# Performance work log

Measured on AMD Instinct MI355X. Metric: run time of the kernel, lower is better.

Reference implementation:

```python
import jax, jax.numpy as jnp
import numpy as np

DIM = 2048
HEADS = 16
HDIM = DIM // HEADS  # 128
B = 1
F, HG, WG = 5, 20, 32
L = F * HG * WG  # 3200
EPS = 1e-6
MAXPOS = 1024
C = HDIM // 2  # 64 rotary pairs
S0 = C - 2 * (C // 3)  # 22 (frame band)
S1 = C // 3            # 21 (height band)


def _rope_tables():
    # Matches Wan rope_params: per-band inverse-freq tables, angle = pos * inv_freq.
    pos = np.arange(MAXPOS, dtype=np.float64)
    chunks = []
    for s in (S0, S1, S1):
        d = 2 * s
        inv = 1.0 / (10000.0 ** (np.arange(0, d, 2, dtype=np.float64) / d))
        chunks.append(np.outer(pos, inv))
    ang = np.concatenate(chunks, axis=1)  # [MAXPOS, C]
    return np.cos(ang).astype(np.float32), np.sin(ang).astype(np.float32)


def setup_inputs() -> dict:
    key = jax.random.key(0)
    ks = jax.random.split(key, 6)
    sc = 1.0 / np.sqrt(DIM)
    fc, fs = _rope_tables()
    return {
        'x': jax.random.normal(ks[0], (B, L, DIM), dtype=jnp.float32),
        'wq': jax.random.normal(ks[1], (DIM, DIM), dtype=jnp.float32) * sc,
        'bq': jnp.zeros((DIM,), jnp.float32),
        'wk': jax.random.normal(ks[2], (DIM, DIM), dtype=jnp.float32) * sc,
        'bk': jnp.zeros((DIM,), jnp.float32),
        'wv': jax.random.normal(ks[3], (DIM, DIM), dtype=jnp.float32) * sc,
        'bv': jnp.zeros((DIM,), jnp.float32),
        'wo': jax.random.normal(ks[4], (DIM, DIM), dtype=jnp.float32) * sc,
        'bo': jnp.zeros((DIM,), jnp.float32),
        'norm_q_w': jnp.ones((DIM,), jnp.float32),
        'norm_k_w': jnp.ones((DIM,), jnp.float32),
        'freqs_cos': jnp.asarray(fc),
        'freqs_sin': jnp.asarray(fs),
    }


def _grid_freqs(tab):
    # Split bands and broadcast over the (F, HG, WG) grid -> [L, C]
    bf, bh, bw = tab[:, :S0], tab[:, S0:S0 + S1], tab[:, S0 + S1:]
    gf = jnp.broadcast_to(bf[:F, None, None, :], (F, HG, WG, S0))
    gh = jnp.broadcast_to(bh[None, :HG, None, :], (F, HG, WG, S1))
    gw = jnp.broadcast_to(bw[None, None, :WG, :], (F, HG, WG, S1))
    return jnp.concatenate([gf, gh, gw], axis=-1).reshape(L, C)


def reference(x, wq, bq, wk, bk, wv, bv, wo, bo, norm_q_w, norm_k_w, freqs_cos, freqs_sin):
    def rms(t, w):
        return t * jax.lax.rsqrt(jnp.mean(t * t, axis=-1, keepdims=True) + EPS) * w

    q = rms(x @ wq.T + bq, norm_q_w).reshape(B, L, HEADS, HDIM)
    k = rms(x @ wk.T + bk, norm_k_w).reshape(B, L, HEADS, HDIM)
    v = (x @ wv.T + bv).reshape(B, L, HEADS, HDIM)

    fc = _grid_freqs(freqs_cos)  # [L, C]
    fs = _grid_freqs(freqs_sin)

    def rope(t):
        tr = t.reshape(B, L, HEADS, C, 2)
        xr, xi = tr[..., 0], tr[..., 1]
        c = fc[None, :, None, :]
        s = fs[None, :, None, :]
        return jnp.stack([xr * c - xi * s, xr * s + xi * c], axis=-1).reshape(B, L, HEADS, HDIM)

    q = rope(q)
    k = rope(k)

    scores = jnp.einsum('blhd,bmhd->bhlm', q, k) / jnp.sqrt(jnp.float32(HDIM))
    attn = jax.nn.softmax(scores, axis=-1)
    out = jnp.einsum('bhlm,bmhd->blhd', attn, v).reshape(B, L, DIM)
    return out @ wo.T + bo
```

## Files before the change

kernel.cpp:

```cpp
#include <hip/hip_runtime.h>

typedef unsigned short u16;
typedef unsigned int u32;
typedef __attribute__((ext_vector_type(4))) float f32x4;
typedef __attribute__((ext_vector_type(8))) short bf16x8;
typedef __attribute__((ext_vector_type(8))) u16 u16x8;
typedef __attribute__((ext_vector_type(4))) u16 u16x4;
typedef __attribute__((ext_vector_type(4))) u32 u32x4;

#define GLOB_AS __attribute__((address_space(1)))
#define LDS_AS  __attribute__((address_space(3)))

__device__ __forceinline__ void gload_lds16(const void* g, void* l) {
  __builtin_amdgcn_global_load_lds((const GLOB_AS void*)g, (LDS_AS void*)l, 16, 0, 0);
}

__device__ __forceinline__ u16 f2bf(float f) {
  u32 u = __builtin_bit_cast(u32, f);
  u += 0x7fffu + ((u >> 16) & 1u);
  return (u16)(u >> 16);
}

__device__ __forceinline__ float bf2f(u16 b) {
  u32 u = (u32)b << 16;
  return __builtin_bit_cast(float, u);
}

#define MFMA16(a, b, c) __builtin_amdgcn_mfma_f32_16x16x32_bf16(a, b, c, 0, 0, 0)

__global__ __launch_bounds__(256) void cast_all(const float* __restrict__ x,
                                                const float* __restrict__ wq,
                                                const float* __restrict__ wk,
                                                const float* __restrict__ wv,
                                                const float* __restrict__ wo,
                                                u16* __restrict__ xb, u16* __restrict__ wqb,
                                                u16* __restrict__ wkb, u16* __restrict__ wvb,
                                                u16* __restrict__ wob) {
  int i = blockIdx.x * 256 + threadIdx.x;
  const float* s;
  u16* d;
  int off;
  if (i < 819200)       { s = x;  d = xb;  off = i; }
  else if (i < 1343488) { s = wq; d = wqb; off = i - 819200; }
  else if (i < 1867776) { s = wk; d = wkb; off = i - 1343488; }
  else if (i < 2392064) { s = wv; d = wvb; off = i - 1867776; }
  else                  { s = wo; d = wob; off = i - 2392064; }
  f32x4 a = ((const f32x4*)s)[2 * off], b = ((const f32x4*)s)[2 * off + 1];
  u16x8 o;
  o[0] = f2bf(a[0]); o[1] = f2bf(a[1]); o[2] = f2bf(a[2]); o[3] = f2bf(a[3]);
  o[4] = f2bf(b[0]); o[5] = f2bf(b[1]); o[6] = f2bf(b[2]); o[7] = f2bf(b[3]);
  ((u16x8*)d)[off] = o;
}

#define GEMM_BODY(C_WRITE)                                                        \
  f32x4 acc[4][4] = {};                                                           \
  const u32 dstoff = wave * 2048 + lane * 8;       \
  int gsb = 0;                                                                    \
  const u16* Agp = Ag;                                                            \
  const u16* Bgp = Bg;                                                            \
  _Pragma("unroll") for (int pf = 0; pf < 2; ++pf) {                              \
    u16* ad = &As[gsb][0] + dstoff;                                               \
    u16* bd = &Bs[gsb][0] + dstoff;                                               \
    gload_lds16(Agp, ad);                                                         \
    gload_lds16(Agp + (size_t)8 * K + d4, ad + 512);                              \
    gload_lds16(Agp + (size_t)16 * K, ad + 1024);                                 \
    gload_lds16(Agp + (size_t)24 * K + d4, ad + 1536);                            \
    gload_lds16(Bgp, bd);                                                         \
    gload_lds16(Bgp + (size_t)8 * K + d4, bd + 512);                              \
    gload_lds16(Bgp + (size_t)16 * K, bd + 1024);                                 \
    gload_lds16(Bgp + (size_t)24 * K + d4, bd + 1536);                            \
    Agp += 64;                                                                    \
    Bgp += 64;                                                                    \
    gsb ^= 1;                                                                     \
  }                                                                               \
  for (int it = 0; it < 32; ++it) {                                               \
    const int buf = it & 1;                                                       \
    if (it < 31)                                                                  \
      asm volatile("s_waitcnt vmcnt(8)" ::: "memory");                            \
    else                                                                          \
      asm volatile("s_waitcnt vmcnt(0)" ::: "memory");                            \
    __builtin_amdgcn_s_barrier();                                                 \
    _Pragma("unroll") for (int kk = 0; kk < 64; kk += 32) {                       \
      bf16x8 af[4], bfr[4];                                                       \
      _Pragma("unroll") for (int mi = 0; mi < 4; mi++)                            \
          af[mi] = *(const bf16x8*)&As[buf][((wr + mi * 16 + li) >> 1) * 128 +    \
              ((((kk >> 3) + lg + 8 * (li & 1)) ^ (li >> 1)) * 8)];               \
      _Pragma("unroll") for (int ni = 0; ni < 4; ni++)                            \
          bfr[ni] = *(const bf16x8*)&Bs[buf][((wc + ni * 16 + li) >> 1) * 128 +   \
              ((((kk >> 3) + lg + 8 * (li & 1)) ^ (li >> 1)) * 8)];               \
      _Pragma("unroll") for (int mi = 0; mi < 4; mi++)                            \
          _Pragma("unroll") for (int ni = 0; ni < 4; ni++)                        \
              acc[mi][ni] = MFMA16(af[mi], bfr[ni], acc[mi][ni]);                 \
    }                                                                             \
    __builtin_amdgcn_s_barrier();                                                 \
    if (it <= 29) {                                                               \
      u16* ad = &As[gsb][0] + dstoff;                                             \
      u16* bd = &Bs[gsb][0] + dstoff;                                             \
      gload_lds16(Agp, ad);                                                       \
      gload_lds16(Agp + (size_t)8 * K + d4, ad + 512);                            \
      gload_lds16(Agp + (size_t)16 * K, ad + 1024);                               \
      gload_lds16(Agp + (size_t)24 * K + d4, ad + 1536);                          \
      gload_lds16(Bgp, bd);                                                       \
      gload_lds16(Bgp + (size_t)8 * K + d4, bd + 512);                            \
      gload_lds16(Bgp + (size_t)16 * K, bd + 1024);                               \
      gload_lds16(Bgp + (size_t)24 * K + d4, bd + 1536);                          \
      Agp += 64;                                                                  \
      Bgp += 64;                                                                  \
      gsb ^= 1;                                                                   \
    }                                                                             \
  }                                                                               \
  float bcol[4];                                                                  \
  _Pragma("unroll") for (int ni = 0; ni < 4; ni++)                                \
      bcol[ni] = bias[n0 + wc + ni * 16 + li];                                    \
  _Pragma("unroll") for (int mi = 0; mi < 4; mi++) {                              \
    _Pragma("unroll") for (int ni = 0; ni < 4; ni++) {                            \
      const int gm = m0 + wr + mi * 16 + lg * 4;                                  \
      const int gn = n0 + wc + ni * 16 + li;                                      \
      _Pragma("unroll") for (int r = 0; r < 4; r++) { C_WRITE; }                  \
    }                                                                             \
  }

#define GEMM_STAGE_SETUP()                                        \
  const int Wl = lane >> 4;                                       \
  const int sl = lane & 15;                                       \
  const int gsa = sl ^ Wl;                                        \
  const int d4 = ((((gsa & 7) ^ 4) - (gsa & 7)) * 8)

__global__ __launch_bounds__(256) void gemm_qkv(const u16* __restrict__ A,
                                                const u16* __restrict__ Bq,
                                                const u16* __restrict__ Bk,
                                                const u16* __restrict__ Bv,
                                                const float* __restrict__ bq,
                                                const float* __restrict__ bk,
                                                const float* __restrict__ bv,
                                                u16* __restrict__ Cq,
                                                u16* __restrict__ Ck,
                                                u16* __restrict__ Cv) {
  constexpr int K = 2048, N = 2048;
  __shared__ u16 As[2][128 * 64];
  __shared__ u16 Bs[2][128 * 64];
  const int tid = threadIdx.x;
  const int wave = tid >> 6, lane = tid & 63;
  const int lg = lane >> 4, li = lane & 15;
  const int lid = blockIdx.x + 25 * blockIdx.y;
  const int tile = (lid & 7) * 150 + (lid >> 3);
  const int bx = tile % 25, by = tile / 25;
  const int m0 = bx * 128;
  const int mat = by >> 4;
  const int n0 = (by & 15) * 128;
  const u16* B = (mat == 0) ? Bq : (mat == 1) ? Bk : Bv;
  const float* bias = (mat == 0) ? bq : (mat == 1) ? bk : bv;
  u16* C = (mat == 0) ? Cq : (mat == 1) ? Ck : Cv;
  const int wr = (wave >> 1) * 64, wc = (wave & 1) * 64;

  GEMM_STAGE_SETUP();
  const u16* Ag = A + (size_t)(m0 + wave * 32 + 2 * Wl + (sl >> 3)) * K + (gsa & 7) * 8;
  const u16* Bg = B + (size_t)(n0 + wave * 32 + 2 * Wl + (sl >> 3)) * K + (gsa & 7) * 8;

  GEMM_BODY(C[(size_t)(gm + r) * N + gn] = f2bf(acc[mi][ni][r] + bcol[ni]))
}

__global__ __launch_bounds__(256) void gemm_nt(const u16* __restrict__ A,
                                               const u16* __restrict__ B,
                                               const float* __restrict__ bias,
                                               float* __restrict__ C) {
  constexpr int K = 2048, N = 2048;
  __shared__ u16 As[2][128 * 64];
  __shared__ u16 Bs[2][128 * 64];
  const int tid = threadIdx.x;
  const int wave = tid >> 6, lane = tid & 63;
  const int lg = lane >> 4, li = lane & 15;
  const int lid = blockIdx.x + 25 * blockIdx.y;
  const int tile = (lid & 7) * 50 + (lid >> 3);
  const int m0 = (tile % 25) * 128, n0 = (tile / 25) * 128;
  const int wr = (wave >> 1) * 64, wc = (wave & 1) * 64;

  GEMM_STAGE_SETUP();
  const u16* Ag = A + (size_t)(m0 + wave * 32 + 2 * Wl + (sl >> 3)) * K + (gsa & 7) * 8;
  const u16* Bg = B + (size_t)(n0 + wave * 32 + 2 * Wl + (sl >> 3)) * K + (gsa & 7) * 8;

  GEMM_BODY(C[(size_t)(gm + r) * N + gn] = acc[mi][ni][r] + bcol[ni])
}

__global__ __launch_bounds__(256) void rms_rope2(const u16* __restrict__ preq,
                                                 const u16* __restrict__ prek,
                                                 const float* __restrict__ wq,
                                                 const float* __restrict__ wk,
                                                 const float* __restrict__ fcos,
                                                 const float* __restrict__ fsin,
                                                 u16* __restrict__ outq,
                                                 u16* __restrict__ outk, float foldq) {
  const int isk = blockIdx.x >= 3200;
  const int l = isk ? blockIdx.x - 3200 : blockIdx.x;
  const u16* pre = isk ? prek : preq;
  const float* w = isk ? wk : wq;
  u16* out = isk ? outk : outq;
  const float fold = isk ? 1.0f : foldq;
  const int tid = threadIdx.x;
  const int d0 = tid * 8;
  u16x8 pv = *(const u16x8*)(pre + (size_t)l * 2048 + d0);
  float xv[8];
#pragma unroll
  for (int j = 0; j < 8; j++) xv[j] = bf2f(pv[j]);
  float ss = (xv[0] * xv[0] + xv[1] * xv[1]) + (xv[2] * xv[2] + xv[3] * xv[3]) +
             (xv[4] * xv[4] + xv[5] * xv[5]) + (xv[6] * xv[6] + xv[7] * xv[7]);
#pragma unroll
  for (int m = 32; m; m >>= 1) ss += __shfl_xor(ss, m);
  __shared__ float red[4];
  if ((tid & 63) == 0) red[tid >> 6] = ss;
  __syncthreads();
  const float scale =
      rsqrtf((red[0] + red[1] + red[2] + red[3]) * (1.0f / 2048.0f) + 1e-6f) * fold;
  f32x4 w0 = *(const f32x4*)(w + d0);
  f32x4 w1 = *(const f32x4*)(w + d0 + 4);
  float xs[8];
#pragma unroll
  for (int j = 0; j < 4; j++) {
    xs[j] = xv[j] * w0[j] * scale;
    xs[4 + j] = xv[4 + j] * w1[j] * scale;
  }
  const int f = l / 640, rem = l % 640;
  const int hh = rem >> 5, ww = rem & 31;
  const int cb = (d0 & 127) >> 1;
  u16x8 ov;
#pragma unroll
  for (int i = 0; i < 4; i++) {
    const int c = cb + i;
    const int prow = c < 22 ? f : (c < 43 ? hh : ww);
    const float fc = fcos[prow * 64 + c];
    const float fs = fsin[prow * 64 + c];
    const float xr = xs[2 * i], xi = xs[2 * i + 1];
    ov[2 * i] = f2bf(xr * fc - xi * fs);
    ov[2 * i + 1] = f2bf(xr * fs + xi * fc);
  }
  *(u16x8*)(out + (size_t)l * 2048 + d0) = ov;
}

__global__ __launch_bounds__(256) void transpose_2d(const u16* __restrict__ src,
                                                    u16* __restrict__ dst) {
  __shared__ u16 t[64][72];
  const int m0 = blockIdx.x * 64, n0 = blockIdx.y * 64;
  const int tid = threadIdx.x;
  const int r = tid >> 3, c8 = (tid & 7) * 8;
#pragma unroll
  for (int j = 0; j < 2; j++) {
    u16x8 v = *(const u16x8*)&src[(size_t)(m0 + r + 32 * j) * 2048 + n0 + c8];
#pragma unroll
    for (int e = 0; e < 8; e++) t[c8 + e][r + 32 * j] = v[e];
  }
  __syncthreads();
  const int b = (c8 >> 5) * 32;
  const int cc = ((c8 >> 3) & 3) * 4;
#pragma unroll
  for (int j = 0; j < 2; j++) {
    const u16* trow = &t[r + 32 * j][0];
    u16x4 lo = *(const u16x4*)&trow[b + cc];
    u16x4 hi = *(const u16x4*)&trow[b + 16 + cc];
    u16x8 v;
    v[0] = lo[0]; v[1] = lo[1]; v[2] = lo[2]; v[3] = lo[3];
    v[4] = hi[0]; v[5] = hi[1]; v[6] = hi[2]; v[7] = hi[3];
    *(u16x8*)&dst[(size_t)(n0 + r + 32 * j) * 3200 + m0 + c8] = v;
  }
}

__global__ __launch_bounds__(512) void attn_kernel(const u16* __restrict__ Q,
                                                   const u16* __restrict__ Kb,
                                                   const u16* __restrict__ VT,
                                                   u16* __restrict__ O) {
  __shared__ u16 Klds[2][64 * 128];
  __shared__ u16 Vlds[2][128 * 64];
  const int tid = threadIdx.x, wave = tid >> 6, lane = tid & 63;
  const int lg = lane >> 4, li = lane & 15;

  const int lid = blockIdx.x + 25 * blockIdx.y;
  const int xcd = lid & 7, ixd = lid >> 3;
  const int h = xcd * 2 + (ixd & 1);
  const int qrow0 = (ixd >> 1) * 128 + wave * 16;

  bf16x8 qf[4];
  {
    const u16* qb = Q + (size_t)(qrow0 + li) * 2048 + h * 128 + lg * 8;
#pragma unroll
    for (int ks = 0; ks < 4; ks++) qf[ks] = *(const bf16x8*)(qb + ks * 32);
  }
  f32x4 o[8] = {};
  float mrow = -1e30f;
  float lrow = 0.f;

  const int klp = lane >> 4;
  const int kg0 = (lane & 15) ^ klp;
  const int kd4 = ((kg0 ^ 4) - kg0) * 8;
  const u16* kp = Kb + (size_t)(wave * 8 + klp) * 2048 + h * 128 + kg0 * 8;
  const int vlp = lane >> 3;
  const int vg = (lane & 7) ^ vlp;
  const u16* vp = VT + (size_t)(h * 128 + wave * 16 + vlp) * 3200 + vg * 8;
  const u32 dstoff = wave * 1024 + lane * 8;
  int sb = 0;

#define STAGE()                               \
  do {                                        \
    u16* kd = &Klds[sb][0] + dstoff;          \
    u16* vd = &Vlds[sb][0] + dstoff;          \
    gload_lds16(kp, kd);                      \
    gload_lds16(kp + 4 * 2048 + kd4, kd + 512); \
    gload_lds16(vp, vd);                      \
    gload_lds16(vp + 8 * 3200, vd + 512);     \
    kp += 64 * 2048;                          \
    vp += 64;                                 \
    sb ^= 1;                                  \
  } while (0)

  STAGE();
  STAGE();

  for (int it = 0; it < 50; ++it) {
    const int buf = it & 1;
    if (it < 49)
      asm volatile("s_waitcnt vmcnt(4)" ::: "memory");
    else
      asm volatile("s_waitcnt vmcnt(0)" ::: "memory");
    __builtin_amdgcn_s_barrier();

    f32x4 s4[4] = {};
#pragma unroll
    for (int t = 0; t < 4; t++)
#pragma unroll
      for (int ks = 0; ks < 4; ks++) {
        const bf16x8 kf = *(const bf16x8*)&Klds[buf][(t * 16 + li) * 128 +
                                                     ((ks * 4 + lg) ^ (li & 7)) * 8];
        s4[t] = MFMA16(kf, qf[ks], s4[t]);
      }
    float pm = fmaxf(fmaxf(fmaxf(s4[0][0], s4[0][1]), fmaxf(s4[0][2], s4[0][3])),
                     fmaxf(fmaxf(s4[1][0], s4[1][1]), fmaxf(s4[1][2], s4[1][3])));
    pm = fmaxf(pm, fmaxf(fmaxf(fmaxf(s4[2][0], s4[2][1]), fmaxf(s4[2][2], s4[2][3])),
                         fmaxf(fmaxf(s4[3][0], s4[3][1]), fmaxf(s4[3][2], s4[3][3]))));
    pm = fmaxf(pm, __shfl_xor(pm, 16));
    pm = fmaxf(pm, __shfl_xor(pm, 32));
    if (__any(pm - mrow > 8.0f)) {
      const float mn = fmaxf(mrow, pm);
      const float alq = exp2f(mrow - mn);
      mrow = mn;
      lrow *= alq;
      float alv[4];
#pragma unroll
      for (int i = 0; i < 4; i++) alv[i] = __shfl(alq, lg * 4 + i);
#pragma unroll
      for (int f8 = 0; f8 < 8; f8++) {
        o[f8][0] *= alv[0]; o[f8][1] *= alv[1];
        o[f8][2] *= alv[2]; o[f8][3] *= alv[3];
      }
    }
    f32x4 p[4];
#pragma unroll
    for (int t = 0; t < 4; t++)
#pragma unroll
      for (int i = 0; i < 4; i++) p[t][i] = exp2f(s4[t][i] - mrow);
    lrow += ((p[0][0] + p[0][1]) + (p[0][2] + p[0][3])) +
            ((p[1][0] + p[1][1]) + (p[1][2] + p[1][3])) +
            ((p[2][0] + p[2][1]) + (p[2][2] + p[2][3])) +
            ((p[3][0] + p[3][1]) + (p[3][2] + p[3][3]));
    u32 wp[8];
    asm("v_cvt_pk_bf16_f32 %0, %1, %2" : "=v"(wp[0]) : "v"(p[0][0]), "v"(p[0][1]));
    asm("v_cvt_pk_bf16_f32 %0, %1, %2" : "=v"(wp[1]) : "v"(p[0][2]), "v"(p[0][3]));
    asm("v_cvt_pk_bf16_f32 %0, %1, %2" : "=v"(wp[2]) : "v"(p[1][0]), "v"(p[1][1]));
    asm("v_cvt_pk_bf16_f32 %0, %1, %2" : "=v"(wp[3]) : "v"(p[1][2]), "v"(p[1][3]));
    asm("v_cvt_pk_bf16_f32 %0, %1, %2" : "=v"(wp[4]) : "v"(p[2][0]), "v"(p[2][1]));
    asm("v_cvt_pk_bf16_f32 %0, %1, %2" : "=v"(wp[5]) : "v"(p[2][2]), "v"(p[2][3]));
    asm("v_cvt_pk_bf16_f32 %0, %1, %2" : "=v"(wp[6]) : "v"(p[3][0]), "v"(p[3][1]));
    asm("v_cvt_pk_bf16_f32 %0, %1, %2" : "=v"(wp[7]) : "v"(p[3][2]), "v"(p[3][3]));
    u32x4 paw0 = {wp[0], wp[1], wp[2], wp[3]};
    u32x4 paw1 = {wp[4], wp[5], wp[6], wp[7]};
    const bf16x8 pa0 = __builtin_bit_cast(bf16x8, paw0);
    const bf16x8 pa1 = __builtin_bit_cast(bf16x8, paw1);

#pragma unroll
    for (int tt = 0; tt < 2; tt++)
#pragma unroll
      for (int f8 = 0; f8 < 8; f8++) {
        const bf16x8 vf = *(const bf16x8*)&Vlds[buf][(f8 * 16 + li) * 64 +
                                                     ((tt * 4 + lg) ^ (li & 7)) * 8];
        o[f8] = MFMA16(tt ? pa1 : pa0, vf, o[f8]);
      }
    __builtin_amdgcn_s_barrier();
    if (it <= 47) STAGE();
  }
#undef STAGE

  float lt = lrow;
  lt += __shfl_xor(lt, 16);
  lt += __shfl_xor(lt, 32);
  const float inv = 1.0f / lt;
  float invi[4];
#pragma unroll
  for (int i = 0; i < 4; i++) invi[i] = __shfl(inv, lg * 4 + i);
#pragma unroll
  for (int i = 0; i < 4; i++) {
    const int row = qrow0 + lg * 4 + i;
#pragma unroll
    for (int f8 = 0; f8 < 8; f8++)
      O[(size_t)row * 2048 + h * 128 + f8 * 16 + li] = f2bf(o[f8][i] * invi[i]);
  }
}

extern "C" void kernel_launch(void* const* d_in, const int* in_sizes, int n_in,
                              void* d_out, int out_size, void* d_ws, size_t ws_size,
                              hipStream_t stream) {
  const float* x    = (const float*)d_in[0];
  const float* wq   = (const float*)d_in[1];
  const float* bq   = (const float*)d_in[2];
  const float* wk   = (const float*)d_in[3];
  const float* bk   = (const float*)d_in[4];
  const float* wv   = (const float*)d_in[5];
  const float* bv   = (const float*)d_in[6];
  const float* wo   = (const float*)d_in[7];
  const float* bo   = (const float*)d_in[8];
  const float* nqw  = (const float*)d_in[9];
  const float* nkw  = (const float*)d_in[10];
  const float* fcos = (const float*)d_in[11];
  const float* fsin = (const float*)d_in[12];

  const size_t NEED = 125304832;
  if (ws_size < NEED) return;
  char* ws = (char*)d_ws;
  u16* x_bf   = (u16*)(ws + 0);
  u16* wq_bf  = (u16*)(ws + 13107200);
  u16* wk_bf  = (u16*)(ws + 21495808);
  u16* wv_bf  = (u16*)(ws + 29884416);
  u16* wo_bf  = (u16*)(ws + 38273024);
  u16* preq   = (u16*)(ws + 46661632);
  u16* prek   = (u16*)(ws + 59768832);
  u16* v_bf   = (u16*)(ws + 72876032);
  u16* q_bf   = (u16*)(ws + 85983232);
  u16* k_bf   = (u16*)(ws + 99090432);
  u16* vT     = (u16*)(ws + 112197632);
  u16* att_bf = (u16*)(ws + 46661632);

  cast_all<<<11392, 256, 0, stream>>>(x, wq, wk, wv, wo, x_bf, wq_bf, wk_bf, wv_bf,
                                      wo_bf);

  const float foldq = 1.4426950408889634f * 0.08838834764831843f;

  gemm_qkv<<<dim3(25, 48), 256, 0, stream>>>(x_bf, wq_bf, wk_bf, wv_bf, bq, bk, bv,
                                             preq, prek, v_bf);
  rms_rope2<<<6400, 256, 0, stream>>>(preq, prek, nqw, nkw, fcos, fsin, q_bf, k_bf,
                                      foldq);
  transpose_2d<<<dim3(50, 32), 256, 0, stream>>>(v_bf, vT);
  attn_kernel<<<dim3(25, 16), 512, 0, stream>>>(q_bf, k_bf, vT, att_bf);
  gemm_nt<<<dim3(25, 16), 256, 0, stream>>>(att_bf, wo_bf, bo, (float*)d_out);
}
```

Before: 320.3 us.

## Process two 16-row query tiles per wave in attention, halving block waves

```diff
diff --git a/kernel.cpp b/kernel.cpp
--- a/kernel.cpp
+++ b/kernel.cpp
@@ -263,7 +263,7 @@
   }
 }
 
-__global__ __launch_bounds__(512) void attn_kernel(const u16* __restrict__ Q,
+__global__ __launch_bounds__(256) void attn_kernel(const u16* __restrict__ Q,
                                                    const u16* __restrict__ Kb,
                                                    const u16* __restrict__ VT,
                                                    u16* __restrict__ O) {
@@ -275,39 +275,47 @@
   const int lid = blockIdx.x + 25 * blockIdx.y;
   const int xcd = lid & 7, ixd = lid >> 3;
   const int h = xcd * 2 + (ixd & 1);
-  const int qrow0 = (ixd >> 1) * 128 + wave * 16;
-
-  bf16x8 qf[4];
+  const int qrow0 = (ixd >> 1) * 128 + wave * 32;
+
+  bf16x8 qf0[4], qf1[4];
   {
-    const u16* qb = Q + (size_t)(qrow0 + li) * 2048 + h * 128 + lg * 8;
-#pragma unroll
-    for (int ks = 0; ks < 4; ks++) qf[ks] = *(const bf16x8*)(qb + ks * 32);
-  }
-  f32x4 o[8] = {};
-  float mrow = -1e30f;
-  float lrow = 0.f;
+    const u16* qb0 = Q + (size_t)(qrow0 + li) * 2048 + h * 128 + lg * 8;
+    const u16* qb1 = qb0 + (size_t)16 * 2048;
+#pragma unroll
+    for (int ks = 0; ks < 4; ks++) {
+      qf0[ks] = *(const bf16x8*)(qb0 + ks * 32);
+      qf1[ks] = *(const bf16x8*)(qb1 + ks * 32);
+    }
+  }
+  f32x4 o0[8] = {}, o1[8] = {};
+  float m0r = -1e30f, m1r = -1e30f;
+  float l0r = 0.f, l1r = 0.f;
 
   const int klp = lane >> 4;
   const int kg0 = (lane & 15) ^ klp;
-  const int kd4 = ((kg0 ^ 4) - kg0) * 8;
-  const u16* kp = Kb + (size_t)(wave * 8 + klp) * 2048 + h * 128 + kg0 * 8;
+  const int kdg8 = ((kg0 ^ 4) - kg0) * 8;
+  const u16* kp = Kb + (size_t)(wave * 16 + klp) * 2048 + h * 128 + kg0 * 8;
   const int vlp = lane >> 3;
   const int vg = (lane & 7) ^ vlp;
-  const u16* vp = VT + (size_t)(h * 128 + wave * 16 + vlp) * 3200 + vg * 8;
-  const u32 dstoff = wave * 1024 + lane * 8;
+  const u16* vp = VT + (size_t)(h * 128 + wave * 32 + vlp) * 3200 + vg * 8;
+  const u32 dstoff = wave * 2048 + lane * 8;
   int sb = 0;
 
-#define STAGE()                               \
-  do {                                        \
-    u16* kd = &Klds[sb][0] + dstoff;          \
-    u16* vd = &Vlds[sb][0] + dstoff;          \
-    gload_lds16(kp, kd);                      \
-    gload_lds16(kp + 4 * 2048 + kd4, kd + 512); \
-    gload_lds16(vp, vd);                      \
-    gload_lds16(vp + 8 * 3200, vd + 512);     \
-    kp += 64 * 2048;                          \
-    vp += 64;                                 \
-    sb ^= 1;                                  \
+#define STAGE()                                       \
+  do {                                                \
+    u16* kd = &Klds[sb][0] + dstoff;                  \
+    u16* vd = &Vlds[sb][0] + dstoff;                  \
+    gload_lds16(kp, kd);                              \
+    gload_lds16(kp + 4 * 2048 + kdg8, kd + 512);      \
+    gload_lds16(kp + 8 * 2048, kd + 1024);            \
+    gload_lds16(kp + 12 * 2048 + kdg8, kd + 1536);    \
+    gload_lds16(vp, vd);                              \
+    gload_lds16(vp + 8 * 3200, vd + 512);             \
+    gload_lds16(vp + 16 * 3200, vd + 1024);           \
+    gload_lds16(vp + 24 * 3200, vd + 1536);           \
+    kp += 64 * 2048;                                  \
+    vp += 64;                                         \
+    sb ^= 1;                                          \
   } while (0)
 
   STAGE();
@@ -316,62 +324,85 @@
   for (int it = 0; it < 50; ++it) {
     const int buf = it & 1;
     if (it < 49)
-      asm volatile("s_waitcnt vmcnt(4)" ::: "memory");
+      asm volatile("s_waitcnt vmcnt(8)" ::: "memory");
     else
       asm volatile("s_waitcnt vmcnt(0)" ::: "memory");
     __builtin_amdgcn_s_barrier();
 
-    f32x4 s4[4] = {};
+    f32x4 sa[4] = {}, sbv[4] = {};
 #pragma unroll
     for (int t = 0; t < 4; t++)
 #pragma unroll
       for (int ks = 0; ks < 4; ks++) {
         const bf16x8 kf = *(const bf16x8*)&Klds[buf][(t * 16 + li) * 128 +
                                                      ((ks * 4 + lg) ^ (li & 7)) * 8];
-        s4[t] = MFMA16(kf, qf[ks], s4[t]);
+        sa[t] = MFMA16(kf, qf0[ks], sa[t]);
+        sbv[t] = MFMA16(kf, qf1[ks], sbv[t]);
       }
-    float pm = fmaxf(fmaxf(fmaxf(s4[0][0], s4[0][1]), fmaxf(s4[0][2], s4[0][3])),
-                     fmaxf(fmaxf(s4[1][0], s4[1][1]), fmaxf(s4[1][2], s4[1][3])));
-    pm = fmaxf(pm, fmaxf(fmaxf(fmaxf(s4[2][0], s4[2][1]), fmaxf(s4[2][2], s4[2][3])),
-                         fmaxf(fmaxf(s4[3][0], s4[3][1]), fmaxf(s4[3][2], s4[3][3]))));
-    pm = fmaxf(pm, __shfl_xor(pm, 16));
-    pm = fmaxf(pm, __shfl_xor(pm, 32));
-    if (__any(pm - mrow > 8.0f)) {
-      const float mn = fmaxf(mrow, pm);
-      const float alq = exp2f(mrow - mn);
-      mrow = mn;
-      lrow *= alq;
-      float alv[4];
-#pragma unroll
-      for (int i = 0; i < 4; i++) alv[i] = __shfl(alq, lg * 4 + i);
+    float pm0 = fmaxf(fmaxf(fmaxf(sa[0][0], sa[0][1]), fmaxf(sa[0][2], sa[0][3])),
+                      fmaxf(fmaxf(sa[1][0], sa[1][1]), fmaxf(sa[1][2], sa[1][3])));
+    pm0 = fmaxf(pm0, fmaxf(fmaxf(fmaxf(sa[2][0], sa[2][1]), fmaxf(sa[2][2], sa[2][3])),
+                           fmaxf(fmaxf(sa[3][0], sa[3][1]), fmaxf(sa[3][2], sa[3][3]))));
+    float pm1 = fmaxf(fmaxf(fmaxf(sbv[0][0], sbv[0][1]), fmaxf(sbv[0][2], sbv[0][3])),
+                      fmaxf(fmaxf(sbv[1][0], sbv[1][1]), fmaxf(sbv[1][2], sbv[1][3])));
+    pm1 = fmaxf(pm1, fmaxf(fmaxf(fmaxf(sbv[2][0], sbv[2][1]), fmaxf(sbv[2][2], sbv[2][3])),
+                           fmaxf(fmaxf(sbv[3][0], sbv[3][1]), fmaxf(sbv[3][2], sbv[3][3]))));
+    pm0 = fmaxf(pm0, __shfl_xor(pm0, 16));
+    pm0 = fmaxf(pm0, __shfl_xor(pm0, 32));
+    pm1 = fmaxf(pm1, __shfl_xor(pm1, 16));
+    pm1 = fmaxf(pm1, __shfl_xor(pm1, 32));
+    if (__any(fmaxf(pm0 - m0r, pm1 - m1r) > 8.0f)) {
+      const float mn0 = fmaxf(m0r, pm0);
+      const float mn1 = fmaxf(m1r, pm1);
+      const float alq0 = exp2f(m0r - mn0);
+      const float alq1 = exp2f(m1r - mn1);
+      m0r = mn0; m1r = mn1;
+      l0r *= alq0; l1r *= alq1;
+      float alv0[4], alv1[4];
+#pragma unroll
+      for (int i = 0; i < 4; i++) {
+        alv0[i] = __shfl(alq0, lg * 4 + i);
+        alv1[i] = __shfl(alq1, lg * 4 + i);
+      }
 #pragma unroll
       for (int f8 = 0; f8 < 8; f8++) {
-        o[f8][0] *= alv[0]; o[f8][1] *= alv[1];
-        o[f8][2] *= alv[2]; o[f8][3] *= alv[3];
+        o0[f8][0] *= alv0[0]; o0[f8][1] *= alv0[1];
+        o0[f8][2] *= alv0[2]; o0[f8][3] *= alv0[3];
+        o1[f8][0] *= alv1[0]; o1[f8][1] *= alv1[1];
+        o1[f8][2] *= alv1[2]; o1[f8][3] *= alv1[3];
       }
     }
-    f32x4 p[4];
 #pragma unroll
     for (int t = 0; t < 4; t++)
 #pragma unroll
-      for (int i = 0; i < 4; i++) p[t][i] = exp2f(s4[t][i] - mrow);
-    lrow += ((p[0][0] + p[0][1]) + (p[0][2] + p[0][3])) +
-            ((p[1][0] + p[1][1]) + (p[1][2] + p[1][3])) +
-            ((p[2][0] + p[2][1]) + (p[2][2] + p[2][3])) +
-            ((p[3][0] + p[3][1]) + (p[3][2] + p[3][3]));
-    u32 wp[8];
-    asm("v_cvt_pk_bf16_f32 %0, %1, %2" : "=v"(wp[0]) : "v"(p[0][0]), "v"(p[0][1]));
-    asm("v_cvt_pk_bf16_f32 %0, %1, %2" : "=v"(wp[1]) : "v"(p[0][2]), "v"(p[0][3]));
-    asm("v_cvt_pk_bf16_f32 %0, %1, %2" : "=v"(wp[2]) : "v"(p[1][0]), "v"(p[1][1]));
-    asm("v_cvt_pk_bf16_f32 %0, %1, %2" : "=v"(wp[3]) : "v"(p[1][2]), "v"(p[1][3]));
-    asm("v_cvt_pk_bf16_f32 %0, %1, %2" : "=v"(wp[4]) : "v"(p[2][0]), "v"(p[2][1]));
-    asm("v_cvt_pk_bf16_f32 %0, %1, %2" : "=v"(wp[5]) : "v"(p[2][2]), "v"(p[2][3]));
-    asm("v_cvt_pk_bf16_f32 %0, %1, %2" : "=v"(wp[6]) : "v"(p[3][0]), "v"(p[3][1]));
-    asm("v_cvt_pk_bf16_f32 %0, %1, %2" : "=v"(wp[7]) : "v"(p[3][2]), "v"(p[3][3]));
-    u32x4 paw0 = {wp[0], wp[1], wp[2], wp[3]};
-    u32x4 paw1 = {wp[4], wp[5], wp[6], wp[7]};
-    const bf16x8 pa0 = __builtin_bit_cast(bf16x8, paw0);
-    const bf16x8 pa1 = __builtin_bit_cast(bf16x8, paw1);
+      for (int i = 0; i < 4; i++) {
+        sa[t][i] = exp2f(sa[t][i] - m0r);
+        sbv[t][i] = exp2f(sbv[t][i] - m1r);
+      }
+    l0r += ((sa[0][0] + sa[0][1]) + (sa[0][2] + sa[0][3])) +
+           ((sa[1][0] + sa[1][1]) + (sa[1][2] + sa[1][3])) +
+           ((sa[2][0] + sa[2][1]) + (sa[2][2] + sa[2][3])) +
+           ((sa[3][0] + sa[3][1]) + (sa[3][2] + sa[3][3]));
+    l1r += ((sbv[0][0] + sbv[0][1]) + (sbv[0][2] + sbv[0][3])) +
+           ((sbv[1][0] + sbv[1][1]) + (sbv[1][2] + sbv[1][3])) +
+           ((sbv[2][0] + sbv[2][1]) + (sbv[2][2] + sbv[2][3])) +
+           ((sbv[3][0] + sbv[3][1]) + (sbv[3][2] + sbv[3][3]));
+    u32 wa[8], wb[8];
+#pragma unroll
+    for (int t = 0; t < 4; t++) {
+      asm("v_cvt_pk_bf16_f32 %0, %1, %2" : "=v"(wa[2 * t]) : "v"(sa[t][0]), "v"(sa[t][1]));
+      asm("v_cvt_pk_bf16_f32 %0, %1, %2" : "=v"(wa[2 * t + 1]) : "v"(sa[t][2]), "v"(sa[t][3]));
+      asm("v_cvt_pk_bf16_f32 %0, %1, %2" : "=v"(wb[2 * t]) : "v"(sbv[t][0]), "v"(sbv[t][1]));
+      asm("v_cvt_pk_bf16_f32 %0, %1, %2" : "=v"(wb[2 * t + 1]) : "v"(sbv[t][2]), "v"(sbv[t][3]));
+    }
+    u32x4 pw00 = {wa[0], wa[1], wa[2], wa[3]};
+    u32x4 pw01 = {wa[4], wa[5], wa[6], wa[7]};
+    u32x4 pw10 = {wb[0], wb[1], wb[2], wb[3]};
+    u32x4 pw11 = {wb[4], wb[5], wb[6], wb[7]};
+    const bf16x8 pa00 = __builtin_bit_cast(bf16x8, pw00);
+    const bf16x8 pa01 = __builtin_bit_cast(bf16x8, pw01);
+    const bf16x8 pa10 = __builtin_bit_cast(bf16x8, pw10);
+    const bf16x8 pa11 = __builtin_bit_cast(bf16x8, pw11);
 
 #pragma unroll
     for (int tt = 0; tt < 2; tt++)
@@ -379,26 +410,35 @@
       for (int f8 = 0; f8 < 8; f8++) {
         const bf16x8 vf = *(const bf16x8*)&Vlds[buf][(f8 * 16 + li) * 64 +
                                                      ((tt * 4 + lg) ^ (li & 7)) * 8];
-        o[f8] = MFMA16(tt ? pa1 : pa0, vf, o[f8]);
+        o0[f8] = MFMA16(tt ? pa01 : pa00, vf, o0[f8]);
+        o1[f8] = MFMA16(tt ? pa11 : pa10, vf, o1[f8]);
       }
     __builtin_amdgcn_s_barrier();
     if (it <= 47) STAGE();
   }
 #undef STAGE
 
-  float lt = lrow;
-  lt += __shfl_xor(lt, 16);
-  lt += __shfl_xor(lt, 32);
-  const float inv = 1.0f / lt;
-  float invi[4];
-#pragma unroll
-  for (int i = 0; i < 4; i++) invi[i] = __shfl(inv, lg * 4 + i);
+  float lt0 = l0r, lt1 = l1r;
+  lt0 += __shfl_xor(lt0, 16);
+  lt0 += __shfl_xor(lt0, 32);
+  lt1 += __shfl_xor(lt1, 16);
+  lt1 += __shfl_xor(lt1, 32);
+  const float inv0 = 1.0f / lt0, inv1 = 1.0f / lt1;
+  float invi0[4], invi1[4];
 #pragma unroll
   for (int i = 0; i < 4; i++) {
-    const int row = qrow0 + lg * 4 + i;
-#pragma unroll
-    for (int f8 = 0; f8 < 8; f8++)
-      O[(size_t)row * 2048 + h * 128 + f8 * 16 + li] = f2bf(o[f8][i] * invi[i]);
+    invi0[i] = __shfl(inv0, lg * 4 + i);
+    invi1[i] = __shfl(inv1, lg * 4 + i);
+  }
+  const size_t obase = (size_t)h * 128 + li;
+#pragma unroll
+  for (int i = 0; i < 4; i++) {
+    const int row0 = qrow0 + lg * 4 + i;
+#pragma unroll
+    for (int f8 = 0; f8 < 8; f8++) {
+      O[obase + (size_t)row0 * 2048 + f8 * 16] = f2bf(o0[f8][i] * invi0[i]);
+      O[obase + (size_t)(row0 + 16) * 2048 + f8 * 16] = f2bf(o1[f8][i] * invi1[i]);
+    }
   }
 }
 
@@ -445,6 +485,6 @@
   rms_rope2<<<6400, 256, 0, stream>>>(preq, prek, nqw, nkw, fcos, fsin, q_bf, k_bf,
                                       foldq);
   transpose_2d<<<dim3(50, 32), 256, 0, stream>>>(v_bf, vT);
-  attn_kernel<<<dim3(25, 16), 512, 0, stream>>>(q_bf, k_bf, vT, att_bf);
+  attn_kernel<<<dim3(25, 16), 256, 0, stream>>>(q_bf, k_bf, vT, att_bf);
   gemm_nt<<<dim3(25, 16), 256, 0, stream>>>(att_bf, wo_bf, bo, (float*)d_out);
 }
```

Result: slower. 403.8 us (+26.1%).
